# Kernel optimization log

Hardware: AMD Instinct MI355X
Metric: run time of the kernel (lower is better)

## Reference

```python
import jax, jax.numpy as jnp
import numpy as np

B, L, D_MODEL, H = 2, 1920, 512, 8
DEPTH = D_MODEL // H
MAX_REL = 1921


def skew(t):
    """Huang et al. 2018 skew: pad, reshape, slice. t: (..., L, L)."""
    Lq, Lk = t.shape[-2], t.shape[-1]
    padded = jnp.pad(t, [(0, 0)] * (t.ndim - 1) + [(1, 0)])  # (..., Lq, Lk+1)
    s = padded.reshape(-1, Lk + 1, Lq)[:, 1:]                 # drop first row
    return s.reshape(t.shape)


def setup_inputs() -> dict:
    key = jax.random.key(0)
    ks = jax.random.split(key, 12)
    w = lambda k, shp: (jax.random.normal(k, shp, jnp.float32) * 0.02)
    inp = {
        "q": jax.random.normal(ks[0], (B, L, D_MODEL), jnp.float32),
        "k": jax.random.normal(ks[1], (B, L, D_MODEL), jnp.float32),
        "v": jax.random.normal(ks[2], (B, L, D_MODEL), jnp.float32),
        "mask": jnp.triu(jnp.ones((L, L), jnp.float32), k=1)[None, None],  # causal look-ahead
        "Wq": w(ks[3], (D_MODEL, D_MODEL)), "bq": jnp.zeros((D_MODEL,), jnp.float32),
        "Wk": w(ks[4], (D_MODEL, D_MODEL)), "bk": jnp.zeros((D_MODEL,), jnp.float32),
        "Wv": w(ks[5], (D_MODEL, D_MODEL)), "bv": jnp.zeros((D_MODEL,), jnp.float32),
        "E": w(ks[6], (MAX_REL, D_MODEL)),
        "Wo": w(ks[7], (D_MODEL, D_MODEL)), "bo": jnp.zeros((D_MODEL,), jnp.float32),
    }
    return inp


def reference(q, k, v, mask, Wq, bq, Wk, bk, Wv, bv, E, Wo, bo):
    Lk = k.shape[-2]
    qp = q @ Wq + bq
    kp = k @ Wk + bk
    vp = v @ Wv + bv
    # required relative embeddings (max_len >= seq_len branch): rightmost Lk rows
    e = E[MAX_REL - Lk:]                                   # (Lk, d_model)
    # split heads
    qh = qp.reshape(B, -1, H, DEPTH).transpose(0, 2, 1, 3)  # (B,H,Lq,depth)
    kh = kp.reshape(B, Lk, H, DEPTH).transpose(0, 2, 1, 3)
    vh = vp.reshape(B, Lk, H, DEPTH).transpose(0, 2, 1, 3)
    eh = e.reshape(Lk, H, DEPTH).transpose(1, 0, 2)         # (H,Lk,depth)
    QKt = jnp.einsum('bhqd,bhkd->bhqk', qh, kh)
    Srel = skew(jnp.einsum('bhqd,hkd->bhqk', qh, eh))
    logits = (QKt + Srel) / jnp.sqrt(jnp.float32(DEPTH))
    logits = logits + mask * (-1e9)
    attn = jax.nn.softmax(logits, axis=-1)                  # (B,H,Lq,Lk)
    out = jnp.einsum('bhqk,bhkd->bhqd', attn, vh)
    out = out.transpose(0, 2, 1, 3).reshape(B, -1, D_MODEL)
    out = out @ Wo + bo
    return out, attn
```

## Files before the change

### kernel.cpp

```cpp
#include <hip/hip_runtime.h>

typedef unsigned short u16;
typedef short s16x8 __attribute__((ext_vector_type(8)));
typedef float f32x4 __attribute__((ext_vector_type(4)));

#define MFMA_BF16(a, b, c) __builtin_amdgcn_mfma_f32_16x16x32_bf16((a), (b), (c), 0, 0, 0)

#define L_SEQ 1920
#define DM    512
#define NH    8

__device__ __forceinline__ u16 f2b(float f) {
  union { float f; unsigned u; } a; a.f = f;
  unsigned u = a.u;
  u += 0x7fffu + ((u >> 16) & 1u);
  return (u16)(u >> 16);
}
__device__ __forceinline__ float b2f(u16 h) {
  union { unsigned u; float f; } a; a.u = ((unsigned)h) << 16;
  return a.f;
}
__device__ __forceinline__ float rmax16(float x) {
  x = fmaxf(x, __shfl_xor(x, 1));
  x = fmaxf(x, __shfl_xor(x, 2));
  x = fmaxf(x, __shfl_xor(x, 4));
  x = fmaxf(x, __shfl_xor(x, 8));
  return x;
}
__device__ __forceinline__ float rsum16(float x) {
  x += __shfl_xor(x, 1);
  x += __shfl_xor(x, 2);
  x += __shfl_xor(x, 4);
  x += __shfl_xor(x, 8);
  return x;
}

__global__ __launch_bounds__(256) void cvtE_kernel(const float* __restrict__ E,
                                                   u16* __restrict__ Ec) {
  const int i = (blockIdx.x * 256 + threadIdx.x) * 8;
  if (i < 983552) {
    float4 a = *(const float4*)(E + i);
    float4 b = *(const float4*)(E + i + 4);
    ushort4 ua; ua.x = f2b(a.x); ua.y = f2b(a.y); ua.z = f2b(a.z); ua.w = f2b(a.w);
    ushort4 ub; ub.x = f2b(b.x); ub.y = f2b(b.y); ub.z = f2b(b.z); ub.w = f2b(b.w);
    *(ushort4*)(Ec + i)     = ua;
    *(ushort4*)(Ec + i + 4) = ub;
  }
}

__global__ __launch_bounds__(256) void wtrans_kernel(
    const float* __restrict__ Wq, const float* __restrict__ Wk,
    const float* __restrict__ Wv, const float* __restrict__ Wo,
    u16* __restrict__ Wqt, u16* __restrict__ Wkt,
    u16* __restrict__ Wvt, u16* __restrict__ Wot) {
  const float* W; u16* Wt;
  if (blockIdx.z == 0)      { W = Wq; Wt = Wqt; }
  else if (blockIdx.z == 1) { W = Wk; Wt = Wkt; }
  else if (blockIdx.z == 2) { W = Wv; Wt = Wvt; }
  else                      { W = Wo; Wt = Wot; }
  const int k0 = blockIdx.y * 64, n0 = blockIdx.x * 64;
  __shared__ u16 T[64][72];
  const int r = threadIdx.x >> 2, c = (threadIdx.x & 3) * 16;
#pragma unroll
  for (int i = 0; i < 4; ++i) {
    float4 f = *(const float4*)(W + (size_t)(k0 + r) * 512 + n0 + c + i * 4);
    ushort4 u; u.x = f2b(f.x); u.y = f2b(f.y); u.z = f2b(f.z); u.w = f2b(f.w);
    *(ushort4*)&T[r][c + i * 4] = u;
  }
  __syncthreads();
  u16 tmp[16];
#pragma unroll
  for (int i = 0; i < 16; ++i) tmp[i] = T[c + i][r];
  u16* dst = Wt + (size_t)(n0 + r) * 512 + k0 + c;
  *(uint4*)dst       = *(uint4*)tmp;
  *(uint4*)(dst + 8) = *(uint4*)(tmp + 8);
}

template<bool ABF, bool OBF>
__device__ __forceinline__ void gemm512_body(const void* Ap, const u16* Wt,
                                             const float* bias, void* Cp) {
  __shared__ u16 As[128][40];
  __shared__ u16 Bs[128][40];
  const int tid  = threadIdx.x;
  const int wv   = tid >> 6, lane = tid & 63, quad = lane >> 4, l16 = lane & 15;
  const int wr   = wv >> 1, wc = wv & 1;
  const int row0 = blockIdx.x * 128, n0 = blockIdx.y * 128;

  f32x4 acc[4][4];
#pragma unroll
  for (int i = 0; i < 4; ++i)
#pragma unroll
    for (int j = 0; j < 4; ++j) acc[i][j] = {0.f, 0.f, 0.f, 0.f};

  for (int kt = 0; kt < 16; ++kt) {
    const int k0 = kt * 32;
    {
      const int r = tid >> 1, cs = (tid & 1) * 16;
      if constexpr (ABF) {
        const u16* src = (const u16*)Ap + (size_t)(row0 + r) * 512 + k0 + cs;
        *(uint4*)&As[r][cs]     = *(const uint4*)src;
        *(uint4*)&As[r][cs + 8] = *(const uint4*)(src + 8);
      } else {
        const float* src = (const float*)Ap + (size_t)(row0 + r) * 512 + k0 + cs;
#pragma unroll
        for (int i = 0; i < 4; ++i) {
          float4 f = *(const float4*)(src + i * 4);
          ushort4 uu; uu.x = f2b(f.x); uu.y = f2b(f.y); uu.z = f2b(f.z); uu.w = f2b(f.w);
          *(ushort4*)&As[r][cs + i * 4] = uu;
        }
      }
    }
    {
      const int r = tid >> 1, cs = (tid & 1) * 16;
      const u16* src = Wt + (size_t)(n0 + r) * 512 + k0 + cs;
      *(uint4*)&Bs[r][cs]     = *(const uint4*)src;
      *(uint4*)&Bs[r][cs + 8] = *(const uint4*)(src + 8);
    }
    __syncthreads();
    s16x8 af[4], bfr[4];
#pragma unroll
    for (int i = 0; i < 4; ++i) af[i]  = *(const s16x8*)&As[wr * 64 + i * 16 + l16][quad * 8];
#pragma unroll
    for (int i = 0; i < 4; ++i) bfr[i] = *(const s16x8*)&Bs[wc * 64 + i * 16 + l16][quad * 8];
#pragma unroll
    for (int am = 0; am < 4; ++am)
#pragma unroll
      for (int bn = 0; bn < 4; ++bn)
        acc[am][bn] = MFMA_BF16(af[am], bfr[bn], acc[am][bn]);
    __syncthreads();
  }

#pragma unroll
  for (int am = 0; am < 4; ++am)
#pragma unroll
    for (int bn = 0; bn < 4; ++bn)
#pragma unroll
      for (int r = 0; r < 4; ++r) {
        const int row = row0 + wr * 64 + am * 16 + quad * 4 + r;
        const int col = n0 + wc * 64 + bn * 16 + l16;
        float v = acc[am][bn][r] + bias[col];
        if constexpr (OBF) ((u16*)Cp)[(size_t)row * 512 + col] = f2b(v);
        else               ((float*)Cp)[(size_t)row * 512 + col] = v;
      }
}

__global__ __launch_bounds__(256) void proj3_kernel(
    const float* __restrict__ q, const float* __restrict__ k, const float* __restrict__ v,
    const u16* __restrict__ Wqt, const u16* __restrict__ Wkt, const u16* __restrict__ Wvt,
    const float* __restrict__ bq, const float* __restrict__ bk, const float* __restrict__ bv,
    u16* __restrict__ qp, u16* __restrict__ kp, u16* __restrict__ vp) {
  const float* A; const u16* W; const float* bias; u16* C;
  if (blockIdx.z == 0)      { A = q; W = Wqt; bias = bq; C = qp; }
  else if (blockIdx.z == 1) { A = k; W = Wkt; bias = bk; C = kp; }
  else                      { A = v; W = Wvt; bias = bv; C = vp; }
  gemm512_body<false, true>(A, W, bias, C);
}

__global__ __launch_bounds__(256) void outproj_kernel(
    const u16* __restrict__ A, const u16* __restrict__ Wot,
    const float* __restrict__ bo, float* __restrict__ out) {
  gemm512_body<true, false>(A, Wot, bo, out);
}

__global__ __launch_bounds__(256) void flash_kernel(
    const u16* __restrict__ qp, const u16* __restrict__ kp, const u16* __restrict__ vp,
    const u16* __restrict__ Ec, float* __restrict__ attn, u16* __restrict__ oc,
    float* __restrict__ msave, float* __restrict__ mfin, float* __restrict__ sfin) {
  __shared__ u16 Qs[64][72];
  __shared__ u16 Ks[64][72];
  __shared__ u16 Vs[64][72];
  __shared__ u16 Es[128][72];
  __shared__ u16 PW[4][16][136];

  const int h = blockIdx.y, b = blockIdx.z;
  const int tid = threadIdx.x, wv = tid >> 6, lane = tid & 63;
  const int quad = lane >> 4, l16 = lane & 15;
  const int j0 = 48 - wv * 16;
  const int bh = b * NH + h;

  const u16* qb = qp + (size_t)b * L_SEQ * DM + h * 64;
  const u16* kb = kp + (size_t)b * L_SEQ * DM + h * 64;
  const u16* vb = vp + (size_t)b * L_SEQ * DM + h * 64;
  const u16* Eb = Ec + h * 64;

  for (int s = 0; s < 2; ++s) {
    const int qt = (s == 0) ? blockIdx.x : 29 - blockIdx.x;
    const int q0 = qt * 64;
    float* ab = attn + ((size_t)bh * L_SEQ + q0) * L_SEQ;

    {
      const int r = tid >> 2, c = (tid & 3) * 16;
      const u16* src = qb + (size_t)(q0 + r) * DM + c;
      *(uint4*)&Qs[r][c]     = *(const uint4*)src;
      *(uint4*)&Qs[r][c + 8] = *(const uint4*)(src + 8);
    }

    float mr[4], sr[4];
#pragma unroll
    for (int r = 0; r < 4; ++r) { mr[r] = -3.0e38f; sr[r] = 0.f; }
    f32x4 oacc[4];
#pragma unroll
    for (int i = 0; i < 4; ++i) oacc[i] = {0.f, 0.f, 0.f, 0.f};

    for (int kt = 0; kt <= qt; ++kt) {
      const int k0 = kt * 64;
      {
        const int r = tid >> 2, c = (tid & 3) * 16;
        const u16* src = kb + (size_t)(k0 + r) * DM + c;
        *(uint4*)&Ks[r][c]     = *(const uint4*)src;
        *(uint4*)&Ks[r][c + 8] = *(const uint4*)(src + 8);
      }
      {
        const int r = tid >> 2, c = (tid & 3) * 16;
        const u16* src = vb + (size_t)(k0 + r) * DM + c;
        union { uint4 u4[2]; u16 us[16]; } t_;
        t_.u4[0] = *(const uint4*)src;
        t_.u4[1] = *(const uint4*)(src + 8);
#pragma unroll
        for (int i = 0; i < 16; ++i) Vs[c + i][r] = t_.us[i];
      }
      {
        const int j = tid >> 1, c2 = (tid & 1) * 32;
        int rg = k0 + (L_SEQ - 64) - q0 + j;
        rg = rg < 0 ? 0 : (rg > L_SEQ - 1 ? L_SEQ - 1 : rg);
        const u16* src = Eb + (size_t)(1 + rg) * DM + c2;
#pragma unroll
        for (int i = 0; i < 4; ++i)
          *(uint4*)&Es[j][c2 + i * 8] = *(const uint4*)(src + i * 8);
      }
      __syncthreads();

      f32x4 qa[4], ba[5];
#pragma unroll
      for (int i = 0; i < 4; ++i) qa[i] = {0.f, 0.f, 0.f, 0.f};
#pragma unroll
      for (int i = 0; i < 5; ++i) ba[i] = {0.f, 0.f, 0.f, 0.f};
#pragma unroll
      for (int kk = 0; kk < 2; ++kk) {
        s16x8 a = *(const s16x8*)&Qs[wv * 16 + l16][kk * 32 + quad * 8];
#pragma unroll
        for (int t = 0; t < 4; ++t) {
          s16x8 kf = *(const s16x8*)&Ks[t * 16 + l16][kk * 32 + quad * 8];
          qa[t] = MFMA_BF16(a, kf, qa[t]);
        }
#pragma unroll
        for (int u = 0; u < 5; ++u) {
          s16x8 ef = *(const s16x8*)&Es[j0 + u * 16 + l16][kk * 32 + quad * 8];
          ba[u] = MFMA_BF16(a, ef, ba[u]);
        }
      }
#pragma unroll
      for (int u = 0; u < 5; ++u)
#pragma unroll
        for (int r = 0; r < 4; ++r)
          PW[wv][quad * 4 + r][u * 16 + l16] = f2b(ba[u][r]);

      float lg[4][4], Mh[4];
#pragma unroll
      for (int r = 0; r < 4; ++r) {
        const int lr = quad * 4 + r;
        const int qi = wv * 16 + lr;
#pragma unroll
        for (int t = 0; t < 4; ++t) {
          const float srel = b2f(PW[wv][lr][15 - lr + 16 * t + l16]);
          const float v = (qa[t][r] + srel) * 0.125f;
          lg[t][r] = ((k0 + t * 16 + l16) <= (q0 + qi)) ? v : -3.0e38f;
        }
        float m = fmaxf(fmaxf(lg[0][r], lg[1][r]), fmaxf(lg[2][r], lg[3][r]));
        Mh[r] = rmax16(m);
      }

      float Sh[4];
#pragma unroll
      for (int r = 0; r < 4; ++r) {
        const int qi = wv * 16 + quad * 4 + r;
        float ssum = 0.f;
#pragma unroll
        for (int t = 0; t < 4; ++t) {
          const float p = __expf(lg[t][r] - Mh[r]);
          lg[t][r] = p;
          ssum += p;
          ab[(size_t)qi * L_SEQ + k0 + t * 16 + l16] = p;
        }
        Sh[r] = rsum16(ssum);
      }

      float al[4], bt[4];
#pragma unroll
      for (int r = 0; r < 4; ++r) {
        const float mn = fmaxf(mr[r], Mh[r]);
        al[r] = __expf(mr[r] - mn);
        bt[r] = __expf(Mh[r] - mn);
        sr[r] = sr[r] * al[r] + Sh[r] * bt[r];
        mr[r] = mn;
      }
      if (l16 == 0) {
#pragma unroll
        for (int r = 0; r < 4; ++r)
          msave[((size_t)bh * L_SEQ + q0 + wv * 16 + quad * 4 + r) * 32 + kt] = Mh[r];
      }

#pragma unroll
      for (int db = 0; db < 4; ++db)
#pragma unroll
        for (int r = 0; r < 4; ++r) oacc[db][r] *= al[r];
#pragma unroll
      for (int t = 0; t < 4; ++t)
#pragma unroll
        for (int r = 0; r < 4; ++r)
          PW[wv][quad * 4 + r][t * 16 + l16] = f2b(lg[t][r] * bt[r]);
#pragma unroll
      for (int kk = 0; kk < 2; ++kk) {
        s16x8 pa = *(const s16x8*)&PW[wv][l16][kk * 32 + quad * 8];
#pragma unroll
        for (int db = 0; db < 4; ++db) {
          s16x8 vf = *(const s16x8*)&Vs[db * 16 + l16][kk * 32 + quad * 8];
          oacc[db] = MFMA_BF16(pa, vf, oacc[db]);
        }
      }
      __syncthreads();
    }

    for (int zt = qt + 1; zt < 30; ++zt) {
      const int qi = tid >> 2, c = (tid & 3) * 16;
      const float4 z = {0.f, 0.f, 0.f, 0.f};
      float* dst = ab + (size_t)qi * L_SEQ + zt * 64 + c;
      *(float4*)(dst)      = z;
      *(float4*)(dst + 4)  = z;
      *(float4*)(dst + 8)  = z;
      *(float4*)(dst + 12) = z;
    }

#pragma unroll
    for (int r = 0; r < 4; ++r) {
      const float inv = 1.0f / sr[r];
      const int qi = wv * 16 + quad * 4 + r;
#pragma unroll
      for (int db = 0; db < 4; ++db)
        oc[(size_t)(b * L_SEQ + q0 + qi) * DM + h * 64 + db * 16 + l16] =
            f2b(oacc[db][r] * inv);
      if (l16 == 0) {
        const size_t gr = (size_t)bh * L_SEQ + q0 + qi;
        mfin[gr] = mr[r];
        sfin[gr] = sr[r];
      }
    }
  }
}

__global__ __launch_bounds__(256) void fixup_kernel(
    float* __restrict__ attn, const float* __restrict__ msave,
    const float* __restrict__ mfin, const float* __restrict__ sfin) {
  const int r = blockIdx.x, bh = blockIdx.y;
  const int qt = r >> 6;
  const size_t rowidx = (size_t)bh * L_SEQ + r;
  float* row = attn + rowidx * L_SEQ;
  const float mf = mfin[rowidx];
  const float si = 1.0f / sfin[rowidx];
  const float* ms = msave + rowidx * 32;
  const int n4 = (qt + 1) * 16;
  for (int i = threadIdx.x; i < n4; i += 256) {
    const float fac = __expf(ms[i >> 4] - mf) * si;
    float4 v = *(float4*)(row + i * 4);
    v.x *= fac; v.y *= fac; v.z *= fac; v.w *= fac;
    *(float4*)(row + i * 4) = v;
  }
}

extern "C" void kernel_launch(void* const* d_in, const int* in_sizes, int n_in,
                              void* d_out, int out_size, void* d_ws, size_t ws_size,
                              hipStream_t stream) {
  const float* q  = (const float*)d_in[0];
  const float* k  = (const float*)d_in[1];
  const float* v  = (const float*)d_in[2];
  const float* Wq = (const float*)d_in[4];
  const float* bq = (const float*)d_in[5];
  const float* Wk = (const float*)d_in[6];
  const float* bk = (const float*)d_in[7];
  const float* Wv = (const float*)d_in[8];
  const float* bv = (const float*)d_in[9];
  const float* E  = (const float*)d_in[10];
  const float* Wo = (const float*)d_in[11];
  const float* bo = (const float*)d_in[12];

  float* out  = (float*)d_out;
  float* attn = out + (size_t)3840 * 512;

  u16* Wqt = (u16*)d_ws;
  u16* Wkt = Wqt + 262144;
  u16* Wvt = Wkt + 262144;
  u16* Wot = Wvt + 262144;
  u16* Ec  = Wot + 262144;
  u16* qp  = Ec + 983552;
  u16* kp  = qp + 1966080;
  u16* vp  = kp + 1966080;
  u16* oc  = vp + 1966080;
  float* msave = (float*)(oc + 1966080);
  float* mfin  = msave + 983040;
  float* sfin  = mfin + 30720;

  cvtE_kernel<<<481, 256, 0, stream>>>(E, Ec);
  wtrans_kernel<<<dim3(8, 8, 4), 256, 0, stream>>>(Wq, Wk, Wv, Wo, Wqt, Wkt, Wvt, Wot);
  proj3_kernel<<<dim3(30, 4, 3), 256, 0, stream>>>(q, k, v, Wqt, Wkt, Wvt,
                                                   bq, bk, bv, qp, kp, vp);
  flash_kernel<<<dim3(15, 8, 2), 256, 0, stream>>>(qp, kp, vp, Ec, attn, oc,
                                                   msave, mfin, sfin);
  fixup_kernel<<<dim3(1920, 16), 256, 0, stream>>>(attn, msave, mfin, sfin);
  outproj_kernel<<<dim3(30, 4), 256, 0, stream>>>(oc, Wot, bo, out);
}
```

Baseline: 459.9 us.

## Split flash attention into key-chunk blocks with max-free softmax and merge pass

The flash kernel now splits each query tile's key range into chunks of up to six tiles, each handled by its own block, giving 1440 blocks instead of 240. Softmax drops the running max and uses plain exp; bf16 unnormalised probabilities go to a workspace, and a merge kernel sums the partial outputs and row sums. The fixup kernel then writes the full fp32 attention row, including the zeros. V is pre-transposed and the q/k/v inputs are pre-converted to bf16 in separate kernels. This adds kernels and workspace traffic, and skipping the max subtraction risks overflow for large logits.

```diff
diff --git a/kernel.cpp b/kernel.cpp
--- a/kernel.cpp
+++ b/kernel.cpp
@@ -9,6 +9,8 @@
 #define L_SEQ 1920
 #define DM    512
 #define NH    8
+#define CH    6
+#define NCHB  90
 
 __device__ __forceinline__ u16 f2b(float f) {
   union { float f; unsigned u; } a; a.f = f;
@@ -19,13 +21,6 @@
 __device__ __forceinline__ float b2f(u16 h) {
   union { unsigned u; float f; } a; a.u = ((unsigned)h) << 16;
   return a.f;
-}
-__device__ __forceinline__ float rmax16(float x) {
-  x = fmaxf(x, __shfl_xor(x, 1));
-  x = fmaxf(x, __shfl_xor(x, 2));
-  x = fmaxf(x, __shfl_xor(x, 4));
-  x = fmaxf(x, __shfl_xor(x, 8));
-  return x;
 }
 __device__ __forceinline__ float rsum16(float x) {
   x += __shfl_xor(x, 1);
@@ -35,16 +30,24 @@
   return x;
 }
 
-__global__ __launch_bounds__(256) void cvtE_kernel(const float* __restrict__ E,
-                                                   u16* __restrict__ Ec) {
+__global__ __launch_bounds__(256) void cvt_kernel(
+    const float* __restrict__ q, const float* __restrict__ k,
+    const float* __restrict__ v, const float* __restrict__ E,
+    u16* __restrict__ qc, u16* __restrict__ kc,
+    u16* __restrict__ vc, u16* __restrict__ Ec) {
+  const float* src; u16* dst; int n;
+  if (blockIdx.y == 0)      { src = q; dst = qc; n = 1966080; }
+  else if (blockIdx.y == 1) { src = k; dst = kc; n = 1966080; }
+  else if (blockIdx.y == 2) { src = v; dst = vc; n = 1966080; }
+  else                      { src = E; dst = Ec; n = 983552; }
   const int i = (blockIdx.x * 256 + threadIdx.x) * 8;
-  if (i < 983552) {
-    float4 a = *(const float4*)(E + i);
-    float4 b = *(const float4*)(E + i + 4);
+  if (i < n) {
+    float4 a = *(const float4*)(src + i);
+    float4 b = *(const float4*)(src + i + 4);
     ushort4 ua; ua.x = f2b(a.x); ua.y = f2b(a.y); ua.z = f2b(a.z); ua.w = f2b(a.w);
     ushort4 ub; ub.x = f2b(b.x); ub.y = f2b(b.y); ub.z = f2b(b.z); ub.w = f2b(b.w);
-    *(ushort4*)(Ec + i)     = ua;
-    *(ushort4*)(Ec + i + 4) = ub;
+    *(ushort4*)(dst + i)     = ua;
+    *(ushort4*)(dst + i + 4) = ub;
   }
 }
 
@@ -76,8 +79,26 @@
   *(uint4*)(dst + 8) = *(uint4*)(tmp + 8);
 }
 
-template<bool ABF, bool OBF>
-__device__ __forceinline__ void gemm512_body(const void* Ap, const u16* Wt,
+__global__ __launch_bounds__(256) void vtrans_kernel(const u16* __restrict__ vp,
+                                                     u16* __restrict__ vt) {
+  const int bh = blockIdx.y, k0 = blockIdx.x * 64;
+  const int b = bh >> 3, h = bh & 7;
+  __shared__ u16 T[64][72];
+  const int r = threadIdx.x >> 2, c = (threadIdx.x & 3) * 16;
+  const u16* src = vp + (size_t)(b * L_SEQ + k0 + r) * DM + h * 64 + c;
+  *(uint4*)&T[r][c]     = *(const uint4*)src;
+  *(uint4*)&T[r][c + 8] = *(const uint4*)(src + 8);
+  __syncthreads();
+  u16 tmp[16];
+#pragma unroll
+  for (int i = 0; i < 16; ++i) tmp[i] = T[c + i][r];
+  u16* dst = vt + (size_t)bh * 64 * L_SEQ + (size_t)r * L_SEQ + k0 + c;
+  *(uint4*)dst       = *(uint4*)tmp;
+  *(uint4*)(dst + 8) = *(uint4*)(tmp + 8);
+}
+
+template<bool OBF>
+__device__ __forceinline__ void gemm512_body(const u16* Ap, const u16* Wt,
                                              const float* bias, void* Cp) {
   __shared__ u16 As[128][40];
   __shared__ u16 Bs[128][40];
@@ -94,24 +115,13 @@
 
   for (int kt = 0; kt < 16; ++kt) {
     const int k0 = kt * 32;
+    const int r = tid >> 1, cs = (tid & 1) * 16;
     {
-      const int r = tid >> 1, cs = (tid & 1) * 16;
-      if constexpr (ABF) {
-        const u16* src = (const u16*)Ap + (size_t)(row0 + r) * 512 + k0 + cs;
-        *(uint4*)&As[r][cs]     = *(const uint4*)src;
-        *(uint4*)&As[r][cs + 8] = *(const uint4*)(src + 8);
-      } else {
-        const float* src = (const float*)Ap + (size_t)(row0 + r) * 512 + k0 + cs;
-#pragma unroll
-        for (int i = 0; i < 4; ++i) {
-          float4 f = *(const float4*)(src + i * 4);
-          ushort4 uu; uu.x = f2b(f.x); uu.y = f2b(f.y); uu.z = f2b(f.z); uu.w = f2b(f.w);
-          *(ushort4*)&As[r][cs + i * 4] = uu;
-        }
-      }
+      const u16* src = Ap + (size_t)(row0 + r) * 512 + k0 + cs;
+      *(uint4*)&As[r][cs]     = *(const uint4*)src;
+      *(uint4*)&As[r][cs + 8] = *(const uint4*)(src + 8);
     }
     {
-      const int r = tid >> 1, cs = (tid & 1) * 16;
       const u16* src = Wt + (size_t)(n0 + r) * 512 + k0 + cs;
       *(uint4*)&Bs[r][cs]     = *(const uint4*)src;
       *(uint4*)&Bs[r][cs + 8] = *(const uint4*)(src + 8);
@@ -145,27 +155,27 @@
 }
 
 __global__ __launch_bounds__(256) void proj3_kernel(
-    const float* __restrict__ q, const float* __restrict__ k, const float* __restrict__ v,
+    const u16* __restrict__ qc, const u16* __restrict__ kc, const u16* __restrict__ vc,
     const u16* __restrict__ Wqt, const u16* __restrict__ Wkt, const u16* __restrict__ Wvt,
     const float* __restrict__ bq, const float* __restrict__ bk, const float* __restrict__ bv,
     u16* __restrict__ qp, u16* __restrict__ kp, u16* __restrict__ vp) {
-  const float* A; const u16* W; const float* bias; u16* C;
-  if (blockIdx.z == 0)      { A = q; W = Wqt; bias = bq; C = qp; }
-  else if (blockIdx.z == 1) { A = k; W = Wkt; bias = bk; C = kp; }
-  else                      { A = v; W = Wvt; bias = bv; C = vp; }
-  gemm512_body<false, true>(A, W, bias, C);
+  const u16* A; const u16* W; const float* bias; u16* C;
+  if (blockIdx.z == 0)      { A = qc; W = Wqt; bias = bq; C = qp; }
+  else if (blockIdx.z == 1) { A = kc; W = Wkt; bias = bk; C = kp; }
+  else                      { A = vc; W = Wvt; bias = bv; C = vp; }
+  gemm512_body<true>(A, W, bias, C);
 }
 
 __global__ __launch_bounds__(256) void outproj_kernel(
     const u16* __restrict__ A, const u16* __restrict__ Wot,
     const float* __restrict__ bo, float* __restrict__ out) {
-  gemm512_body<true, false>(A, Wot, bo, out);
+  gemm512_body<false>(A, Wot, bo, out);
 }
 
 __global__ __launch_bounds__(256) void flash_kernel(
-    const u16* __restrict__ qp, const u16* __restrict__ kp, const u16* __restrict__ vp,
-    const u16* __restrict__ Ec, float* __restrict__ attn, u16* __restrict__ oc,
-    float* __restrict__ msave, float* __restrict__ mfin, float* __restrict__ sfin) {
+    const u16* __restrict__ qp, const u16* __restrict__ kp, const u16* __restrict__ vt,
+    const u16* __restrict__ Ec, u16* __restrict__ phat,
+    float* __restrict__ opart, float* __restrict__ spart) {
   __shared__ u16 Qs[64][72];
   __shared__ u16 Ks[64][72];
   __shared__ u16 Vs[64][72];
@@ -178,193 +188,188 @@
   const int j0 = 48 - wv * 16;
   const int bh = b * NH + h;
 
+  int qt = 0, c = blockIdx.x;
+  for (;;) { const int n = (qt + CH) / CH; if (c < n) break; c -= n; ++qt; }
+  const int kts = c * CH, kte = min(qt, kts + CH - 1);
+  const int q0 = qt * 64;
+  const size_t gcid = (size_t)bh * NCHB + blockIdx.x;
+
   const u16* qb = qp + (size_t)b * L_SEQ * DM + h * 64;
   const u16* kb = kp + (size_t)b * L_SEQ * DM + h * 64;
-  const u16* vb = vp + (size_t)b * L_SEQ * DM + h * 64;
+  const u16* vtb = vt + (size_t)bh * 64 * L_SEQ;
   const u16* Eb = Ec + h * 64;
-
-  for (int s = 0; s < 2; ++s) {
-    const int qt = (s == 0) ? blockIdx.x : 29 - blockIdx.x;
-    const int q0 = qt * 64;
-    float* ab = attn + ((size_t)bh * L_SEQ + q0) * L_SEQ;
-
+  u16* pb = phat + ((size_t)bh * L_SEQ + q0) * L_SEQ;
+
+  {
+    const int r = tid >> 2, cc = (tid & 3) * 16;
+    const u16* src = qb + (size_t)(q0 + r) * DM + cc;
+    *(uint4*)&Qs[r][cc]     = *(const uint4*)src;
+    *(uint4*)&Qs[r][cc + 8] = *(const uint4*)(src + 8);
+  }
+
+  float sr[4] = {0.f, 0.f, 0.f, 0.f};
+  f32x4 oacc[4];
+#pragma unroll
+  for (int i = 0; i < 4; ++i) oacc[i] = {0.f, 0.f, 0.f, 0.f};
+
+  for (int kt = kts; kt <= kte; ++kt) {
+    const int k0 = kt * 64;
     {
-      const int r = tid >> 2, c = (tid & 3) * 16;
-      const u16* src = qb + (size_t)(q0 + r) * DM + c;
-      *(uint4*)&Qs[r][c]     = *(const uint4*)src;
-      *(uint4*)&Qs[r][c + 8] = *(const uint4*)(src + 8);
-    }
-
-    float mr[4], sr[4];
-#pragma unroll
-    for (int r = 0; r < 4; ++r) { mr[r] = -3.0e38f; sr[r] = 0.f; }
-    f32x4 oacc[4];
-#pragma unroll
-    for (int i = 0; i < 4; ++i) oacc[i] = {0.f, 0.f, 0.f, 0.f};
-
-    for (int kt = 0; kt <= qt; ++kt) {
-      const int k0 = kt * 64;
-      {
-        const int r = tid >> 2, c = (tid & 3) * 16;
-        const u16* src = kb + (size_t)(k0 + r) * DM + c;
-        *(uint4*)&Ks[r][c]     = *(const uint4*)src;
-        *(uint4*)&Ks[r][c + 8] = *(const uint4*)(src + 8);
+      const int r = tid >> 2, cc = (tid & 3) * 16;
+      const u16* src = kb + (size_t)(k0 + r) * DM + cc;
+      *(uint4*)&Ks[r][cc]     = *(const uint4*)src;
+      *(uint4*)&Ks[r][cc + 8] = *(const uint4*)(src + 8);
+    }
+    {
+      const int d = tid >> 2, cc = (tid & 3) * 16;
+      const u16* src = vtb + (size_t)d * L_SEQ + k0 + cc;
+      *(uint4*)&Vs[d][cc]     = *(const uint4*)src;
+      *(uint4*)&Vs[d][cc + 8] = *(const uint4*)(src + 8);
+    }
+    {
+      const int j = tid >> 1, c2 = (tid & 1) * 32;
+      int rg = k0 + (L_SEQ - 64) - q0 + j;
+      rg = rg < 0 ? 0 : (rg > L_SEQ - 1 ? L_SEQ - 1 : rg);
+      const u16* src = Eb + (size_t)(1 + rg) * DM + c2;
+#pragma unroll
+      for (int i = 0; i < 4; ++i)
+        *(uint4*)&Es[j][c2 + i * 8] = *(const uint4*)(src + i * 8);
+    }
+    __syncthreads();
+
+    f32x4 qa[4], ba[5];
+#pragma unroll
+    for (int i = 0; i < 4; ++i) qa[i] = {0.f, 0.f, 0.f, 0.f};
+#pragma unroll
+    for (int i = 0; i < 5; ++i) ba[i] = {0.f, 0.f, 0.f, 0.f};
+#pragma unroll
+    for (int kk = 0; kk < 2; ++kk) {
+      s16x8 a = *(const s16x8*)&Qs[wv * 16 + l16][kk * 32 + quad * 8];
+#pragma unroll
+      for (int t = 0; t < 4; ++t) {
+        s16x8 kf = *(const s16x8*)&Ks[t * 16 + l16][kk * 32 + quad * 8];
+        qa[t] = MFMA_BF16(a, kf, qa[t]);
       }
-      {
-        const int r = tid >> 2, c = (tid & 3) * 16;
-        const u16* src = vb + (size_t)(k0 + r) * DM + c;
-        union { uint4 u4[2]; u16 us[16]; } t_;
-        t_.u4[0] = *(const uint4*)src;
-        t_.u4[1] = *(const uint4*)(src + 8);
-#pragma unroll
-        for (int i = 0; i < 16; ++i) Vs[c + i][r] = t_.us[i];
+#pragma unroll
+      for (int u = 0; u < 5; ++u) {
+        s16x8 ef = *(const s16x8*)&Es[j0 + u * 16 + l16][kk * 32 + quad * 8];
+        ba[u] = MFMA_BF16(a, ef, ba[u]);
       }
-      {
-        const int j = tid >> 1, c2 = (tid & 1) * 32;
-        int rg = k0 + (L_SEQ - 64) - q0 + j;
-        rg = rg < 0 ? 0 : (rg > L_SEQ - 1 ? L_SEQ - 1 : rg);
-        const u16* src = Eb + (size_t)(1 + rg) * DM + c2;
-#pragma unroll
-        for (int i = 0; i < 4; ++i)
-          *(uint4*)&Es[j][c2 + i * 8] = *(const uint4*)(src + i * 8);
+    }
+#pragma unroll
+    for (int u = 0; u < 5; ++u)
+#pragma unroll
+      for (int r = 0; r < 4; ++r)
+        PW[wv][quad * 4 + r][u * 16 + l16] = f2b(ba[u][r]);
+
+    u16 pb16[4][4];
+#pragma unroll
+    for (int r = 0; r < 4; ++r) {
+      const int lr = quad * 4 + r;
+      const int qi = wv * 16 + lr;
+      float ssum = 0.f;
+#pragma unroll
+      for (int t = 0; t < 4; ++t) {
+        const float srel = b2f(PW[wv][lr][15 - lr + 16 * t + l16]);
+        const float v = (qa[t][r] + srel) * 0.125f;
+        const float p = ((k0 + t * 16 + l16) <= (q0 + qi)) ? __expf(v) : 0.f;
+        ssum += p;
+        const u16 pc = f2b(p);
+        pb16[r][t] = pc;
+        pb[(size_t)qi * L_SEQ + k0 + t * 16 + l16] = pc;
       }
-      __syncthreads();
-
-      f32x4 qa[4], ba[5];
-#pragma unroll
-      for (int i = 0; i < 4; ++i) qa[i] = {0.f, 0.f, 0.f, 0.f};
-#pragma unroll
-      for (int i = 0; i < 5; ++i) ba[i] = {0.f, 0.f, 0.f, 0.f};
-#pragma unroll
-      for (int kk = 0; kk < 2; ++kk) {
-        s16x8 a = *(const s16x8*)&Qs[wv * 16 + l16][kk * 32 + quad * 8];
-#pragma unroll
-        for (int t = 0; t < 4; ++t) {
-          s16x8 kf = *(const s16x8*)&Ks[t * 16 + l16][kk * 32 + quad * 8];
-          qa[t] = MFMA_BF16(a, kf, qa[t]);
-        }
-#pragma unroll
-        for (int u = 0; u < 5; ++u) {
-          s16x8 ef = *(const s16x8*)&Es[j0 + u * 16 + l16][kk * 32 + quad * 8];
-          ba[u] = MFMA_BF16(a, ef, ba[u]);
-        }
+      sr[r] += rsum16(ssum);
+    }
+#pragma unroll
+    for (int t = 0; t < 4; ++t)
+#pragma unroll
+      for (int r = 0; r < 4; ++r)
+        PW[wv][quad * 4 + r][t * 16 + l16] = pb16[r][t];
+
+#pragma unroll
+    for (int kk = 0; kk < 2; ++kk) {
+      s16x8 pa = *(const s16x8*)&PW[wv][l16][kk * 32 + quad * 8];
+#pragma unroll
+      for (int db = 0; db < 4; ++db) {
+        s16x8 vf = *(const s16x8*)&Vs[db * 16 + l16][kk * 32 + quad * 8];
+        oacc[db] = MFMA_BF16(pa, vf, oacc[db]);
       }
-#pragma unroll
-      for (int u = 0; u < 5; ++u)
-#pragma unroll
-        for (int r = 0; r < 4; ++r)
-          PW[wv][quad * 4 + r][u * 16 + l16] = f2b(ba[u][r]);
-
-      float lg[4][4], Mh[4];
-#pragma unroll
-      for (int r = 0; r < 4; ++r) {
-        const int lr = quad * 4 + r;
-        const int qi = wv * 16 + lr;
-#pragma unroll
-        for (int t = 0; t < 4; ++t) {
-          const float srel = b2f(PW[wv][lr][15 - lr + 16 * t + l16]);
-          const float v = (qa[t][r] + srel) * 0.125f;
-          lg[t][r] = ((k0 + t * 16 + l16) <= (q0 + qi)) ? v : -3.0e38f;
-        }
-        float m = fmaxf(fmaxf(lg[0][r], lg[1][r]), fmaxf(lg[2][r], lg[3][r]));
-        Mh[r] = rmax16(m);
-      }
-
-      float Sh[4];
-#pragma unroll
-      for (int r = 0; r < 4; ++r) {
-        const int qi = wv * 16 + quad * 4 + r;
-        float ssum = 0.f;
-#pragma unroll
-        for (int t = 0; t < 4; ++t) {
-          const float p = __expf(lg[t][r] - Mh[r]);
-          lg[t][r] = p;
-          ssum += p;
-          ab[(size_t)qi * L_SEQ + k0 + t * 16 + l16] = p;
-        }
-        Sh[r] = rsum16(ssum);
-      }
-
-      float al[4], bt[4];
-#pragma unroll
-      for (int r = 0; r < 4; ++r) {
-        const float mn = fmaxf(mr[r], Mh[r]);
-        al[r] = __expf(mr[r] - mn);
-        bt[r] = __expf(Mh[r] - mn);
-        sr[r] = sr[r] * al[r] + Sh[r] * bt[r];
-        mr[r] = mn;
-      }
-      if (l16 == 0) {
-#pragma unroll
-        for (int r = 0; r < 4; ++r)
-          msave[((size_t)bh * L_SEQ + q0 + wv * 16 + quad * 4 + r) * 32 + kt] = Mh[r];
-      }
-
-#pragma unroll
-      for (int db = 0; db < 4; ++db)
-#pragma unroll
-        for (int r = 0; r < 4; ++r) oacc[db][r] *= al[r];
-#pragma unroll
-      for (int t = 0; t < 4; ++t)
-#pragma unroll
-        for (int r = 0; r < 4; ++r)
-          PW[wv][quad * 4 + r][t * 16 + l16] = f2b(lg[t][r] * bt[r]);
-#pragma unroll
-      for (int kk = 0; kk < 2; ++kk) {
-        s16x8 pa = *(const s16x8*)&PW[wv][l16][kk * 32 + quad * 8];
-#pragma unroll
-        for (int db = 0; db < 4; ++db) {
-          s16x8 vf = *(const s16x8*)&Vs[db * 16 + l16][kk * 32 + quad * 8];
-          oacc[db] = MFMA_BF16(pa, vf, oacc[db]);
-        }
-      }
-      __syncthreads();
-    }
-
-    for (int zt = qt + 1; zt < 30; ++zt) {
-      const int qi = tid >> 2, c = (tid & 3) * 16;
-      const float4 z = {0.f, 0.f, 0.f, 0.f};
-      float* dst = ab + (size_t)qi * L_SEQ + zt * 64 + c;
-      *(float4*)(dst)      = z;
-      *(float4*)(dst + 4)  = z;
-      *(float4*)(dst + 8)  = z;
-      *(float4*)(dst + 12) = z;
-    }
-
-#pragma unroll
-    for (int r = 0; r < 4; ++r) {
-      const float inv = 1.0f / sr[r];
-      const int qi = wv * 16 + quad * 4 + r;
-#pragma unroll
-      for (int db = 0; db < 4; ++db)
-        oc[(size_t)(b * L_SEQ + q0 + qi) * DM + h * 64 + db * 16 + l16] =
-            f2b(oacc[db][r] * inv);
-      if (l16 == 0) {
-        const size_t gr = (size_t)bh * L_SEQ + q0 + qi;
-        mfin[gr] = mr[r];
-        sfin[gr] = sr[r];
-      }
-    }
-  }
+    }
+    __syncthreads();
+  }
+
+  float* op = opart + gcid * 4096;
+#pragma unroll
+  for (int db = 0; db < 4; ++db)
+#pragma unroll
+    for (int r = 0; r < 4; ++r)
+      op[(size_t)(wv * 16 + quad * 4 + r) * 64 + db * 16 + l16] = oacc[db][r];
+  if (l16 == 0) {
+#pragma unroll
+    for (int r = 0; r < 4; ++r)
+      spart[gcid * 64 + wv * 16 + quad * 4 + r] = sr[r];
+  }
+}
+
+__global__ __launch_bounds__(256) void merge_kernel(
+    const float* __restrict__ opart, const float* __restrict__ spart,
+    u16* __restrict__ oc, float* __restrict__ sfin) {
+  const int qt = blockIdx.x, bh = blockIdx.y;
+  const int b = bh >> 3, h = bh & 7;
+  int pre = 0;
+  for (int q2 = 0; q2 < qt; ++q2) pre += (q2 + CH) / CH;
+  const int nc = (qt + CH) / CH;
+  const size_t gc0 = (size_t)bh * NCHB + pre;
+
+  const int qi = threadIdx.x >> 2, ds = (threadIdx.x & 3) * 16;
+  float s = 0.f;
+  float4 o[4] = {{0,0,0,0},{0,0,0,0},{0,0,0,0},{0,0,0,0}};
+  for (int ci = 0; ci < nc; ++ci) {
+    s += spart[(gc0 + ci) * 64 + qi];
+    const float* op = opart + (gc0 + ci) * 4096 + (size_t)qi * 64 + ds;
+#pragma unroll
+    for (int i = 0; i < 4; ++i) {
+      const float4 a = *(const float4*)(op + i * 4);
+      o[i].x += a.x; o[i].y += a.y; o[i].z += a.z; o[i].w += a.w;
+    }
+  }
+  const float inv = 1.0f / s;
+  u16* dst = oc + (size_t)(b * L_SEQ + qt * 64 + qi) * DM + h * 64 + ds;
+#pragma unroll
+  for (int i = 0; i < 4; ++i) {
+    ushort4 u;
+    u.x = f2b(o[i].x * inv); u.y = f2b(o[i].y * inv);
+    u.z = f2b(o[i].z * inv); u.w = f2b(o[i].w * inv);
+    *(ushort4*)(dst + i * 4) = u;
+  }
+  if ((threadIdx.x & 3) == 0) sfin[(size_t)bh * L_SEQ + qt * 64 + qi] = s;
 }
 
 __global__ __launch_bounds__(256) void fixup_kernel(
-    float* __restrict__ attn, const float* __restrict__ msave,
-    const float* __restrict__ mfin, const float* __restrict__ sfin) {
+    const u16* __restrict__ phat, const float* __restrict__ sfin,
+    float* __restrict__ attn) {
   const int r = blockIdx.x, bh = blockIdx.y;
-  const int qt = r >> 6;
+  const int nlow = ((r >> 6) + 1) * 64;
   const size_t rowidx = (size_t)bh * L_SEQ + r;
-  float* row = attn + rowidx * L_SEQ;
-  const float mf = mfin[rowidx];
-  const float si = 1.0f / sfin[rowidx];
-  const float* ms = msave + rowidx * 32;
-  const int n4 = (qt + 1) * 16;
-  for (int i = threadIdx.x; i < n4; i += 256) {
-    const float fac = __expf(ms[i >> 4] - mf) * si;
-    float4 v = *(float4*)(row + i * 4);
-    v.x *= fac; v.y *= fac; v.z *= fac; v.w *= fac;
-    *(float4*)(row + i * 4) = v;
-  }
+  const u16* prow = phat + rowidx * L_SEQ;
+  float* arow = attn + rowidx * L_SEQ;
+  const int g = threadIdx.x;
+  if (g >= 240) return;
+  const int col = g * 8;
+  float4 o0, o1;
+  if (col < nlow) {
+    const float fac = 1.0f / sfin[rowidx];
+    uint4 u = *(const uint4*)(prow + col);
+    o0.x = b2f((u16)(u.x & 0xffff)) * fac;  o0.y = b2f((u16)(u.x >> 16)) * fac;
+    o0.z = b2f((u16)(u.y & 0xffff)) * fac;  o0.w = b2f((u16)(u.y >> 16)) * fac;
+    o1.x = b2f((u16)(u.z & 0xffff)) * fac;  o1.y = b2f((u16)(u.z >> 16)) * fac;
+    o1.z = b2f((u16)(u.w & 0xffff)) * fac;  o1.w = b2f((u16)(u.w >> 16)) * fac;
+  } else {
+    o0 = {0.f, 0.f, 0.f, 0.f};
+    o1 = {0.f, 0.f, 0.f, 0.f};
+  }
+  *(float4*)(arow + col)     = o0;
+  *(float4*)(arow + col + 4) = o1;
 }
 
 extern "C" void kernel_launch(void* const* d_in, const int* in_sizes, int n_in,
@@ -386,7 +391,10 @@
   float* out  = (float*)d_out;
   float* attn = out + (size_t)3840 * 512;
 
-  u16* Wqt = (u16*)d_ws;
+  u16* qc  = (u16*)d_ws;
+  u16* kc  = qc + 1966080;
+  u16* vc  = kc + 1966080;
+  u16* Wqt = vc + 1966080;
   u16* Wkt = Wqt + 262144;
   u16* Wvt = Wkt + 262144;
   u16* Wot = Wvt + 262144;
@@ -394,17 +402,20 @@
   u16* qp  = Ec + 983552;
   u16* kp  = qp + 1966080;
   u16* vp  = kp + 1966080;
-  u16* oc  = vp + 1966080;
-  float* msave = (float*)(oc + 1966080);
-  float* mfin  = msave + 983040;
-  float* sfin  = mfin + 30720;
-
-  cvtE_kernel<<<481, 256, 0, stream>>>(E, Ec);
+  u16* vt  = vp + 1966080;
+  u16* oc  = vt + 1966080;
+  u16* phat = oc + 1966080;
+  float* opart = (float*)(phat + 58982400);
+  float* spart = opart + (size_t)1440 * 4096;
+  float* sfin  = spart + 1440 * 64;
+
+  cvt_kernel<<<dim3(960, 4), 256, 0, stream>>>(q, k, v, E, qc, kc, vc, Ec);
   wtrans_kernel<<<dim3(8, 8, 4), 256, 0, stream>>>(Wq, Wk, Wv, Wo, Wqt, Wkt, Wvt, Wot);
-  proj3_kernel<<<dim3(30, 4, 3), 256, 0, stream>>>(q, k, v, Wqt, Wkt, Wvt,
+  proj3_kernel<<<dim3(30, 4, 3), 256, 0, stream>>>(qc, kc, vc, Wqt, Wkt, Wvt,
                                                    bq, bk, bv, qp, kp, vp);
-  flash_kernel<<<dim3(15, 8, 2), 256, 0, stream>>>(qp, kp, vp, Ec, attn, oc,
-                                                   msave, mfin, sfin);
-  fixup_kernel<<<dim3(1920, 16), 256, 0, stream>>>(attn, msave, mfin, sfin);
+  vtrans_kernel<<<dim3(30, 16), 256, 0, stream>>>(vp, vt);
+  flash_kernel<<<dim3(NCHB, 8, 2), 256, 0, stream>>>(qp, kp, vt, Ec, phat, opart, spart);
+  merge_kernel<<<dim3(30, 16), 256, 0, stream>>>(opart, spart, oc, sfin);
+  fixup_kernel<<<dim3(1920, 16), 256, 0, stream>>>(phat, sfin, attn);
   outproj_kernel<<<dim3(30, 4), 256, 0, stream>>>(oc, Wot, bo, out);
 }
```

Result: faster. 430.7 us (-6.3%).
